# Kernel optimization log

Hardware: AMD Instinct MI355X
Metric: run time of the kernel (lower is better)

## Reference

```python
import jax, jax.numpy as jnp
import numpy as np

DIM = 64       # input/output channels
DHEAD = 16     # channels per head
HEADS = 4
INNER = DHEAD * HEADS  # 64
B, H, W = 4, 256, 256
EPS = 1e-12    # F.normalize eps


def setup_inputs() -> dict:
    key = jax.random.key(0)
    ks = jax.random.split(key, 6)
    x_in = jax.random.normal(ks[0], (B, DIM, H, W), jnp.float32)
    illu_fea_trans = jax.random.normal(ks[1], (B, INNER, H, W), jnp.float32)
    # qkv 1x1 conv (no bias): weight [3*inner, dim]
    w_qkv = jax.random.normal(ks[2], (3 * INNER, DIM), jnp.float32) * 0.05
    # depthwise 3x3 conv: OIHW with I=1, groups = 3*inner
    w_dw = jax.random.normal(ks[3], (3 * INNER, 1, 3, 3), jnp.float32) * 0.1
    # project_out 1x1 conv: [dim, inner]
    w_out = jax.random.normal(ks[4], (DIM, INNER), jnp.float32) * 0.05
    temperature = jnp.ones((HEADS, 1, 1), jnp.float32)
    return {"x_in": x_in, "illu_fea_trans": illu_fea_trans,
            "w_qkv": w_qkv, "w_dw": w_dw, "w_out": w_out,
            "temperature": temperature}


def _l2_normalize(t):
    # F.normalize(t, dim=-1): t / max(||t||_2, eps)
    n = jnp.sqrt(jnp.sum(t * t, axis=-1, keepdims=True))
    return t / jnp.maximum(n, EPS)


def reference(x_in, illu_fea_trans, w_qkv, w_dw, w_out, temperature):
    b, c, h, w = x_in.shape
    # 1x1 conv (pointwise) then depthwise 3x3 conv
    qkv = jnp.einsum('oc,bchw->bohw', w_qkv, x_in)
    qkv = jax.lax.conv_general_dilated(
        qkv, w_dw, window_strides=(1, 1), padding='SAME',
        dimension_numbers=('NCHW', 'OIHW', 'NCHW'),
        feature_group_count=3 * INNER)
    q, k, v = jnp.split(qkv, 3, axis=1)
    # b (n d) h w -> b n d (h w)
    def to_heads(t):
        return t.reshape(b, HEADS, DHEAD, h * w)
    q, k, v, illu = map(to_heads, (q, k, v, illu_fea_trans))
    q = _l2_normalize(q)
    k = _l2_normalize(k)
    # channel-wise attention: [b,n,d,d]
    attn = jnp.einsum('bndL,bneL->bnde', q, k) * temperature[None]
    attn = jax.nn.softmax(attn, axis=-1)
    out = jnp.einsum('bnde,bneL->bndL', attn, v * illu)
    out = out.reshape(b, INNER, h, w)
    return jnp.einsum('oc,bchw->bohw', w_out, out)
```

## Files before the change

### kernel.cpp

```cpp
#include <hip/hip_runtime.h>
#include <math.h>

#define NB 4
#define NC 64
#define NH 256
#define NW 256
#define NL (NH * NW)
#define NHEADS 4

typedef __attribute__((ext_vector_type(8))) short short8;
typedef __attribute__((ext_vector_type(8))) unsigned short ushort8;
typedef __attribute__((ext_vector_type(4))) float f32x4;

#define GRAM_FLOATS 4608
#define MT_OFF_F 8192
#define QKV_PRE_OFF ((size_t)1 << 20)
#define QKV_BYTES ((size_t)192 * NL * NB * 2)
#define QKVDW_OFF (QKV_PRE_OFF + QKV_BYTES)
#define WS_NEEDED (QKVDW_OFF + QKV_BYTES)

__device__ __forceinline__ float bf2f(unsigned short u16) {
    union { unsigned int i; float f; } cv; cv.i = ((unsigned int)u16) << 16; return cv.f;
}
__device__ __forceinline__ unsigned short f2bf(float f) {
    union { float f; unsigned int i; } cv; cv.f = f;
    unsigned int x = cv.i;
    return (unsigned short)((x + 0x7FFFu + ((x >> 16) & 1u)) >> 16);
}

__global__ __launch_bounds__(256) void k1_qkv_mfma(
    const float* __restrict__ x, const float* __restrict__ wqkv,
    unsigned short* __restrict__ qkv)
{
    const int b = blockIdx.z;
    const int og = blockIdx.y;
    const int wave = threadIdx.x >> 6;
    const int lane = threadIdx.x & 63;
    const int ln  = lane & 15;
    const int kb  = (lane >> 4) * 8;
    const int oc0 = og * 64 + wave * 16;
    const int px0 = blockIdx.x * 256;

    short8 wf0, wf1;
    {
        const float* wrow = wqkv + (oc0 + ln) * 64;
        #pragma unroll
        for (int j = 0; j < 8; ++j) {
            wf0[j] = (short)f2bf(wrow[kb + j]);
            wf1[j] = (short)f2bf(wrow[32 + kb + j]);
        }
    }

    const float* xb = x + (size_t)b * NC * NL;
    unsigned short* outp = qkv + (size_t)b * 192 * NL;

    #pragma unroll 2
    for (int it = 0; it < 16; ++it) {
        const int p = px0 + it * 16 + ln;
        short8 xf0, xf1;
        #pragma unroll
        for (int j = 0; j < 8; ++j) {
            xf0[j] = (short)f2bf(xb[(size_t)(kb + j) * NL + p]);
            xf1[j] = (short)f2bf(xb[(size_t)(32 + kb + j) * NL + p]);
        }
        f32x4 acc = {0.f, 0.f, 0.f, 0.f};
        acc = __builtin_amdgcn_mfma_f32_16x16x32_bf16(wf0, xf0, acc, 0, 0, 0);
        acc = __builtin_amdgcn_mfma_f32_16x16x32_bf16(wf1, xf1, acc, 0, 0, 0);
        const int prow = (lane >> 4) * 4;
        #pragma unroll
        for (int r = 0; r < 4; ++r)
            outp[(size_t)(oc0 + prow + r) * NL + p] = f2bf(acc[r]);
    }
}

__global__ __launch_bounds__(256) void k2_dw(
    const unsigned short* __restrict__ qkv, const float* __restrict__ wdw,
    unsigned short* __restrict__ qkvdw)
{
    const int b = blockIdx.z, ch = blockIdx.y;
    const int r = blockIdx.x * 8 + (threadIdx.x >> 5);
    const int cg = threadIdx.x & 31;
    const int c0 = cg * 8;
    const unsigned short* in = qkv + ((size_t)b * 192 + ch) * NL;

    float w[9];
    #pragma unroll
    for (int i = 0; i < 9; ++i) w[i] = wdw[ch * 9 + i];

    float v[3][8], lf[3], rt[3];
    #pragma unroll
    for (int dy = 0; dy < 3; ++dy) {
        const int rr = r + dy - 1;
        const bool valid = (rr >= 0) && (rr < NH);
        const int rc = valid ? rr : r;
        const ushort8 u = *(const ushort8*)(in + rc * NW + c0);
        #pragma unroll
        for (int i = 0; i < 8; ++i) v[dy][i] = valid ? bf2f(u[i]) : 0.f;
        lf[dy] = __shfl_up(v[dy][7], 1);
        rt[dy] = __shfl_down(v[dy][0], 1);
        if (cg == 0)  lf[dy] = 0.f;
        if (cg == 31) rt[dy] = 0.f;
    }

    float acc[8];
    #pragma unroll
    for (int i = 0; i < 8; ++i) {
        float a = 0.f;
        #pragma unroll
        for (int dy = 0; dy < 3; ++dy) {
            const float lv = (i == 0) ? lf[dy] : v[dy][i - 1];
            const float mv = v[dy][i];
            const float rv = (i == 7) ? rt[dy] : v[dy][i + 1];
            a = fmaf(w[dy * 3 + 0], lv, a);
            a = fmaf(w[dy * 3 + 1], mv, a);
            a = fmaf(w[dy * 3 + 2], rv, a);
        }
        acc[i] = a;
    }
    ushort8 o8;
    #pragma unroll
    for (int i = 0; i < 8; ++i) o8[i] = f2bf(acc[i]);
    *(ushort8*)(qkvdw + ((size_t)b * 192 + ch) * NL + r * NW + c0) = o8;
}

__global__ __launch_bounds__(256) void k3_gram(
    const unsigned short* __restrict__ qkvdw, float* __restrict__ gram)
{
    const int b = blockIdx.z, n = blockIdx.y;
    const int wave = threadIdx.x >> 6, lane = threadIdx.x & 63;
    const int p0 = blockIdx.x * 2048 + wave * 512;
    const unsigned short* qrow = qkvdw + ((size_t)b * 192 + n * 16 + (lane & 15)) * NL;
    const unsigned short* krow = qkvdw + ((size_t)b * 192 + 64 + n * 16 + (lane & 15)) * NL;
    const int koff = (lane >> 4) * 8;

    f32x4 acc = {0.f, 0.f, 0.f, 0.f};
    float qq = 0.f, kk = 0.f;
    for (int s = 0; s < 16; ++s) {
        const int p = p0 + s * 32 + koff;
        const short8 a  = *(const short8*)(qrow + p);
        const short8 bb = *(const short8*)(krow + p);
        acc = __builtin_amdgcn_mfma_f32_16x16x32_bf16(a, bb, acc, 0, 0, 0);
        #pragma unroll
        for (int j = 0; j < 8; ++j) {
            const float qv = bf2f((unsigned short)a[j]);
            const float kv = bf2f((unsigned short)bb[j]);
            qq = fmaf(qv, qv, qq);
            kk = fmaf(kv, kv, kk);
        }
    }
    float* gb = gram + (b * NHEADS + n) * 288;
    #pragma unroll
    for (int r = 0; r < 4; ++r)
        atomicAdd(gb + ((lane >> 4) * 4 + r) * 16 + (lane & 15), acc[r]);
    atomicAdd(gb + 256 + (lane & 15), qq);
    atomicAdd(gb + 272 + (lane & 15), kk);
}

__global__ __launch_bounds__(256) void attn_kernel(
    const float* __restrict__ gram, const float* __restrict__ wout,
    const float* __restrict__ temp, float* __restrict__ Mt)
{
    __shared__ float attn_s[NHEADS][16][16];
    const int b = blockIdx.x;
    const int tid = threadIdx.x;

    if (tid < 64) {
        const int n = tid >> 4, d = tid & 15;
        const float* gb = gram + (b * NHEADS + n) * 288;
        const float nq = fmaxf(sqrtf(gb[256 + d]), 1e-12f);
        const float tn = temp[n];
        float lg[16];
        float mx = -3.4e38f;
        #pragma unroll
        for (int e = 0; e < 16; ++e) {
            const float nk = fmaxf(sqrtf(gb[272 + e]), 1e-12f);
            lg[e] = gb[d * 16 + e] / (nq * nk) * tn;
            mx = fmaxf(mx, lg[e]);
        }
        float s = 0.f;
        #pragma unroll
        for (int e = 0; e < 16; ++e) { lg[e] = expf(lg[e] - mx); s += lg[e]; }
        const float inv = 1.0f / s;
        #pragma unroll
        for (int e = 0; e < 16; ++e) attn_s[n][d][e] = lg[e] * inv;
    }
    __syncthreads();

    for (int idx = tid; idx < 4096; idx += 256) {
        const int c = idx >> 6;
        const int o = idx & 63;
        const int n = c >> 4, e = c & 15;
        float acc = 0.f;
        #pragma unroll
        for (int d = 0; d < 16; ++d)
            acc = fmaf(wout[o * 64 + n * 16 + d], attn_s[n][d][e], acc);
        Mt[b * 4096 + idx] = acc;
    }
}

__global__ __launch_bounds__(256) void k5_out(
    const unsigned short* __restrict__ qkvdw, const float* __restrict__ illu,
    const float* __restrict__ Mt, float* __restrict__ out)
{
    const int b = blockIdx.y;
    const int p = blockIdx.x * 256 + threadIdx.x;
    const unsigned short* vp = qkvdw + ((size_t)b * 192 + 128) * NL + p;
    const float* ip = illu + (size_t)b * 64 * NL + p;
    const float* mb = Mt + b * 4096;

    float y[64];
    #pragma unroll
    for (int o = 0; o < 64; ++o) y[o] = 0.f;

    #pragma unroll 4
    for (int c = 0; c < 64; ++c) {
        const float vi = bf2f(vp[(size_t)c * NL]) * ip[(size_t)c * NL];
        const float* m = mb + c * 64;
        #pragma unroll
        for (int o = 0; o < 64; ++o) y[o] = fmaf(m[o], vi, y[o]);
    }

    float* op = out + (size_t)b * 64 * NL + p;
    #pragma unroll
    for (int o = 0; o < 64; ++o) op[(size_t)o * NL] = y[o];
}

__global__ __launch_bounds__(256, 2) void fb_pass1(
    const float* __restrict__ x, const float* __restrict__ wqkv,
    const float* __restrict__ wdw, float* __restrict__ gram)
{
    __shared__ float predw[32][328];
    __shared__ float qk[32][262];
    const int bid = blockIdx.x;
    const int b = bid >> 8;
    const int tile = bid & 255;
    const int y0 = (tile >> 4) << 4;
    const int x0 = (tile & 15) << 4;
    const int tid = threadIdx.x;
    const int iy = tid >> 4, ix = tid & 15;

    for (int n = 0; n < NHEADS; ++n) {
        for (int task = tid; task < 324; task += 256) {
            const int hy = task / 18;
            const int hx = task - hy * 18;
            const int py = y0 + hy - 1;
            const int px = x0 + hx - 1;
            const bool valid = (py >= 0) && (py < NH) && (px >= 0) && (px < NW);
            const float* xp = x + (size_t)b * (NC * NL) + py * NW + px;
            float xr[NC];
            #pragma unroll
            for (int c = 0; c < NC; ++c)
                xr[c] = valid ? xp[(size_t)c * NL] : 0.0f;
            for (int j = 0; j < 16; ++j) {
                const float* wq = wqkv + (n * 16 + j) * NC;
                const float* wk = wqkv + (64 + n * 16 + j) * NC;
                float aq = 0.f, ak = 0.f;
                #pragma unroll
                for (int c = 0; c < NC; ++c) {
                    aq = fmaf(wq[c], xr[c], aq);
                    ak = fmaf(wk[c], xr[c], ak);
                }
                predw[j][task] = aq;
                predw[16 + j][task] = ak;
            }
        }
        __syncthreads();
        {
            const int hp = (iy + 1) * 18 + (ix + 1);
            #pragma unroll
            for (int j = 0; j < 32; ++j) {
                const int ch = (j < 16) ? (n * 16 + j) : (64 + n * 16 + (j - 16));
                const float* wd = wdw + ch * 9;
                float a = 0.f;
                #pragma unroll
                for (int t9 = 0; t9 < 9; ++t9) {
                    const int dy = t9 / 3, dx = t9 - dy * 3;
                    a = fmaf(wd[t9], predw[j][hp + (dy - 1) * 18 + (dx - 1)], a);
                }
                qk[j][tid] = a;
            }
        }
        __syncthreads();
        {
            const int d = tid >> 4, e = tid & 15;
            float acc = 0.f;
            #pragma unroll 8
            for (int p = 0; p < 256; ++p)
                acc = fmaf(qk[d][p], qk[16 + e][p], acc);
            float* gb = gram + ((b * NHEADS + n) * 288);
            atomicAdd(gb + tid, acc);
            if (tid < 32) {
                float s = 0.f;
                #pragma unroll 8
                for (int p = 0; p < 256; ++p) {
                    const float v = qk[tid][p];
                    s = fmaf(v, v, s);
                }
                atomicAdd(gb + 256 + tid, s);
            }
        }
        __syncthreads();
    }
}

__global__ __launch_bounds__(256, 2) void fb_pass2(
    const float* __restrict__ x, const float* __restrict__ illu,
    const float* __restrict__ wqkv, const float* __restrict__ wdw,
    const float* __restrict__ Mt, float* __restrict__ out)
{
    __shared__ float predw[32][328];
    const int bid = blockIdx.x;
    const int b = bid >> 8;
    const int tile = bid & 255;
    const int y0 = (tile >> 4) << 4;
    const int x0 = (tile & 15) << 4;
    const int tid = threadIdx.x;
    const int iy = tid >> 4, ix = tid & 15;
    const int pidx = (y0 + iy) * NW + (x0 + ix);

    float y[64];
    #pragma unroll
    for (int o = 0; o < 64; ++o) y[o] = 0.f;

    for (int cv = 0; cv < 2; ++cv) {
        if (cv) __syncthreads();
        for (int half = 0; half < 2; ++half) {
            for (int task = tid; task < 324; task += 256) {
                const int hy = task / 18;
                const int hx = task - hy * 18;
                const int py = y0 + hy - 1;
                const int px = x0 + hx - 1;
                const bool valid = (py >= 0) && (py < NH) && (px >= 0) && (px < NW);
                const float* xp = x + (size_t)b * (NC * NL) + py * NW + px
                                  + (size_t)(half * 32) * NL;
                float xr[32];
                #pragma unroll
                for (int c = 0; c < 32; ++c)
                    xr[c] = valid ? xp[(size_t)c * NL] : 0.0f;
                for (int j = 0; j < 32; ++j) {
                    const float* wv = wqkv + (128 + cv * 32 + j) * NC + half * 32;
                    float a = 0.f;
                    #pragma unroll
                    for (int c = 0; c < 32; ++c) a = fmaf(wv[c], xr[c], a);
                    if (half == 0) predw[j][task] = a;
                    else           predw[j][task] += a;
                }
            }
        }
        __syncthreads();
        {
            const int hp = (iy + 1) * 18 + (ix + 1);
            for (int j = 0; j < 32; ++j) {
                const int ci = cv * 32 + j;
                const float* wd = wdw + (128 + ci) * 9;
                float a = 0.f;
                #pragma unroll
                for (int t9 = 0; t9 < 9; ++t9) {
                    const int dy = t9 / 3, dx = t9 - dy * 3;
                    a = fmaf(wd[t9], predw[j][hp + (dy - 1) * 18 + (dx - 1)], a);
                }
                const float vi = a * illu[(size_t)(b * 64 + ci) * NL + pidx];
                const float* mrow = Mt + b * 4096 + ci * 64;
                #pragma unroll
                for (int o = 0; o < 64; ++o)
                    y[o] = fmaf(mrow[o], vi, y[o]);
            }
        }
    }
    const size_t obase = (size_t)b * (64 * NL) + pidx;
    #pragma unroll
    for (int o = 0; o < 64; ++o)
        out[obase + (size_t)o * NL] = y[o];
}

extern "C" void kernel_launch(void* const* d_in, const int* in_sizes, int n_in,
                              void* d_out, int out_size, void* d_ws, size_t ws_size,
                              hipStream_t stream)
{
    const float* x    = (const float*)d_in[0];
    const float* illu = (const float*)d_in[1];
    const float* wqkv = (const float*)d_in[2];
    const float* wdw  = (const float*)d_in[3];
    const float* wout = (const float*)d_in[4];
    const float* temp = (const float*)d_in[5];
    float* out = (float*)d_out;
    float* ws  = (float*)d_ws;

    float* gram = ws;
    float* Mt   = ws + MT_OFF_F;

    hipMemsetAsync(gram, 0, GRAM_FLOATS * sizeof(float), stream);

    if (ws_size >= WS_NEEDED) {
        unsigned short* qkv_pre = (unsigned short*)((char*)d_ws + QKV_PRE_OFF);
        unsigned short* qkvdw   = (unsigned short*)((char*)d_ws + QKVDW_OFF);

        k1_qkv_mfma<<<dim3(NL / 256, 3, NB), dim3(256), 0, stream>>>(x, wqkv, qkv_pre);
        k2_dw  <<<dim3(NH / 8, 192, NB), dim3(256), 0, stream>>>(qkv_pre, wdw, qkvdw);
        k3_gram<<<dim3(32, NHEADS, NB),  dim3(256), 0, stream>>>(qkvdw, gram);
        attn_kernel<<<dim3(NB), dim3(256), 0, stream>>>(gram, wout, temp, Mt);
        k5_out <<<dim3(NL / 256, NB),    dim3(256), 0, stream>>>(qkvdw, illu, Mt, out);
    } else {
        fb_pass1<<<dim3(1024), dim3(256), 0, stream>>>(x, wqkv, wdw, gram);
        attn_kernel<<<dim3(NB), dim3(256), 0, stream>>>(gram, wout, temp, Mt);
        fb_pass2<<<dim3(1024), dim3(256), 0, stream>>>(x, illu, wqkv, wdw, Mt, out);
    }
}
```

Before: 358.0 us.

## Move output projection onto bf16 MFMA and prefetch inputs in QKV kernel

The final output kernel, previously a per-thread scalar FMA loop over 64 channels with the mixing matrix read from global memory, now computes the projection with 16x16x32 bf16 MFMA instructions. The mixing matrix is kept in registers as bf16 fragments, and the v*illu product is rounded to bf16. Both the QKV pointwise kernel and the new output kernel software-prefetch the next pixel tile's inputs into registers to overlap loads with compute. The change lowers precision of the output projection and raises register pressure.

Result: slower. 365.5 us (+2.1%).

```diff
diff --git a/kernel.cpp b/kernel.cpp
--- a/kernel.cpp
+++ b/kernel.cpp
@@ -38,6 +38,7 @@
     const int lane = threadIdx.x & 63;
     const int ln  = lane & 15;
     const int kb  = (lane >> 4) * 8;
+    const int prow = (lane >> 4) * 4;
     const int oc0 = og * 64 + wave * 16;
     const int px0 = blockIdx.x * 256;
 
@@ -54,22 +55,44 @@
     const float* xb = x + (size_t)b * NC * NL;
     unsigned short* outp = qkv + (size_t)b * 192 * NL;
 
-    #pragma unroll 2
+    float cur[16];
+    {
+        const int p = px0 + ln;
+        #pragma unroll
+        for (int j = 0; j < 8; ++j) {
+            cur[j]     = xb[(size_t)(kb + j) * NL + p];
+            cur[8 + j] = xb[(size_t)(32 + kb + j) * NL + p];
+        }
+    }
+
+    #pragma unroll
     for (int it = 0; it < 16; ++it) {
-        const int p = px0 + it * 16 + ln;
+        float nxt[16];
+        if (it < 15) {
+            const int pn = px0 + (it + 1) * 16 + ln;
+            #pragma unroll
+            for (int j = 0; j < 8; ++j) {
+                nxt[j]     = xb[(size_t)(kb + j) * NL + pn];
+                nxt[8 + j] = xb[(size_t)(32 + kb + j) * NL + pn];
+            }
+        }
         short8 xf0, xf1;
         #pragma unroll
         for (int j = 0; j < 8; ++j) {
-            xf0[j] = (short)f2bf(xb[(size_t)(kb + j) * NL + p]);
-            xf1[j] = (short)f2bf(xb[(size_t)(32 + kb + j) * NL + p]);
+            xf0[j] = (short)f2bf(cur[j]);
+            xf1[j] = (short)f2bf(cur[8 + j]);
         }
         f32x4 acc = {0.f, 0.f, 0.f, 0.f};
         acc = __builtin_amdgcn_mfma_f32_16x16x32_bf16(wf0, xf0, acc, 0, 0, 0);
         acc = __builtin_amdgcn_mfma_f32_16x16x32_bf16(wf1, xf1, acc, 0, 0, 0);
-        const int prow = (lane >> 4) * 4;
+        const int p = px0 + it * 16 + ln;
         #pragma unroll
         for (int r = 0; r < 4; ++r)
             outp[(size_t)(oc0 + prow + r) * NL + p] = f2bf(acc[r]);
+        if (it < 15) {
+            #pragma unroll
+            for (int j = 0; j < 16; ++j) cur[j] = nxt[j];
+        }
     }
 }
 
@@ -198,31 +221,79 @@
     }
 }
 
-__global__ __launch_bounds__(256) void k5_out(
+__global__ __launch_bounds__(256) void k5_mfma(
     const unsigned short* __restrict__ qkvdw, const float* __restrict__ illu,
     const float* __restrict__ Mt, float* __restrict__ out)
 {
     const int b = blockIdx.y;
-    const int p = blockIdx.x * 256 + threadIdx.x;
-    const unsigned short* vp = qkvdw + ((size_t)b * 192 + 128) * NL + p;
-    const float* ip = illu + (size_t)b * 64 * NL + p;
+    const int wave = threadIdx.x >> 6, lane = threadIdx.x & 63;
+    const int ln = lane & 15;
+    const int kb = (lane >> 4) * 8;
+    const int prow = (lane >> 4) * 4;
+    const int px0 = blockIdx.x * 256 + wave * 64;
+    const unsigned short* vb = qkvdw + ((size_t)b * 192 + 128) * NL;
+    const float* ib = illu + (size_t)b * 64 * NL;
     const float* mb = Mt + b * 4096;
-
-    float y[64];
-    #pragma unroll
-    for (int o = 0; o < 64; ++o) y[o] = 0.f;
-
-    #pragma unroll 4
-    for (int c = 0; c < 64; ++c) {
-        const float vi = bf2f(vp[(size_t)c * NL]) * ip[(size_t)c * NL];
-        const float* m = mb + c * 64;
-        #pragma unroll
-        for (int o = 0; o < 64; ++o) y[o] = fmaf(m[o], vi, y[o]);
-    }
-
-    float* op = out + (size_t)b * 64 * NL + p;
-    #pragma unroll
-    for (int o = 0; o < 64; ++o) op[(size_t)o * NL] = y[o];
+    float* ob = out + (size_t)b * 64 * NL;
+
+    short8 mf0[4], mf1[4];
+    #pragma unroll
+    for (int oc = 0; oc < 4; ++oc) {
+        #pragma unroll
+        for (int j = 0; j < 8; ++j) {
+            mf0[oc][j] = (short)f2bf(mb[(kb + j) * 64 + oc * 16 + ln]);
+            mf1[oc][j] = (short)f2bf(mb[(32 + kb + j) * 64 + oc * 16 + ln]);
+        }
+    }
+
+    unsigned short vcur[16];
+    float icur[16];
+    {
+        const int p = px0 + ln;
+        #pragma unroll
+        for (int j = 0; j < 8; ++j) {
+            vcur[j]     = vb[(size_t)(kb + j) * NL + p];
+            vcur[8 + j] = vb[(size_t)(32 + kb + j) * NL + p];
+            icur[j]     = ib[(size_t)(kb + j) * NL + p];
+            icur[8 + j] = ib[(size_t)(32 + kb + j) * NL + p];
+        }
+    }
+
+    #pragma unroll
+    for (int t = 0; t < 4; ++t) {
+        unsigned short vnx[16];
+        float inx[16];
+        if (t < 3) {
+            const int pn = px0 + (t + 1) * 16 + ln;
+            #pragma unroll
+            for (int j = 0; j < 8; ++j) {
+                vnx[j]     = vb[(size_t)(kb + j) * NL + pn];
+                vnx[8 + j] = vb[(size_t)(32 + kb + j) * NL + pn];
+                inx[j]     = ib[(size_t)(kb + j) * NL + pn];
+                inx[8 + j] = ib[(size_t)(32 + kb + j) * NL + pn];
+            }
+        }
+        short8 bf0, bf1;
+        #pragma unroll
+        for (int j = 0; j < 8; ++j) {
+            bf0[j] = (short)f2bf(bf2f(vcur[j])     * icur[j]);
+            bf1[j] = (short)f2bf(bf2f(vcur[8 + j]) * icur[8 + j]);
+        }
+        const int p = px0 + t * 16 + ln;
+        #pragma unroll
+        for (int oc = 0; oc < 4; ++oc) {
+            f32x4 acc = {0.f, 0.f, 0.f, 0.f};
+            acc = __builtin_amdgcn_mfma_f32_16x16x32_bf16(mf0[oc], bf0, acc, 0, 0, 0);
+            acc = __builtin_amdgcn_mfma_f32_16x16x32_bf16(mf1[oc], bf1, acc, 0, 0, 0);
+            #pragma unroll
+            for (int r = 0; r < 4; ++r)
+                ob[(size_t)(oc * 16 + prow + r) * NL + p] = acc[r];
+        }
+        if (t < 3) {
+            #pragma unroll
+            for (int j = 0; j < 16; ++j) { vcur[j] = vnx[j]; icur[j] = inx[j]; }
+        }
+    }
 }
 
 __global__ __launch_bounds__(256, 2) void fb_pass1(
@@ -399,7 +470,7 @@
         k2_dw  <<<dim3(NH / 8, 192, NB), dim3(256), 0, stream>>>(qkv_pre, wdw, qkvdw);
         k3_gram<<<dim3(32, NHEADS, NB),  dim3(256), 0, stream>>>(qkvdw, gram);
         attn_kernel<<<dim3(NB), dim3(256), 0, stream>>>(gram, wout, temp, Mt);
-        k5_out <<<dim3(NL / 256, NB),    dim3(256), 0, stream>>>(qkvdw, illu, Mt, out);
+        k5_mfma<<<dim3(NL / 256, NB),    dim3(256), 0, stream>>>(qkvdw, illu, Mt, out);
     } else {
         fb_pass1<<<dim3(1024), dim3(256), 0, stream>>>(x, wqkv, wdw, gram);
         attn_kernel<<<dim3(NB), dim3(256), 0, stream>>>(gram, wout, temp, Mt);
```
